# Kernel tuning notes

Hardware: AMD Instinct MI355X
Metric: run time of the kernel (lower is better)

## Reference

```python
import jax, jax.numpy as jnp
import numpy as np

EMBED_DIM = 1024
NUM_HEADS = 16
HEAD_DIM = EMBED_DIM // NUM_HEADS
SCALE = 1.0 / np.sqrt(HEAD_DIM)


def _quant_linear(x, w, b):
    # Per-tensor symmetric int8 quantize -> dequantize -> GEMM (faithful to QuantizedLinear)
    s = jnp.max(jnp.abs(w)) / 127.0
    w_dq = jnp.clip(jnp.round(w / s), -128.0, 127.0) * s
    return jnp.einsum('bse,oe->bso', x, w_dq) + b


def setup_inputs() -> dict:
    key = jax.random.key(0)
    ks = jax.random.split(key, 7)
    B, S, E = 2, 2048, EMBED_DIM
    return {
        'query': jax.random.normal(ks[0], (B, S, E), dtype=jnp.float32),
        'key': jax.random.normal(ks[1], (B, S, E), dtype=jnp.float32),
        'value': jax.random.normal(ks[2], (B, S, E), dtype=jnp.float32),
        'Wq': jax.random.normal(ks[3], (E, E), dtype=jnp.float32) * 0.02,
        'bq': jnp.zeros((E,), dtype=jnp.float32),
        'Wk': jax.random.normal(ks[4], (E, E), dtype=jnp.float32) * 0.02,
        'bk': jnp.zeros((E,), dtype=jnp.float32),
        'Wv': jax.random.normal(ks[5], (E, E), dtype=jnp.float32) * 0.02,
        'bv': jnp.zeros((E,), dtype=jnp.float32),
        'Wo': jax.random.normal(ks[6], (E, E), dtype=jnp.float32) * 0.02,
        'bo': jnp.zeros((E,), dtype=jnp.float32),
    }


def reference(query, key, value, Wq, bq, Wk, bk, Wv, bv, Wo, bo):
    B, S, E = query.shape
    H, D = NUM_HEADS, HEAD_DIM
    Q = _quant_linear(query, Wq, bq).reshape(B, S, H, D).transpose(0, 2, 1, 3)
    K = _quant_linear(key, Wk, bk).reshape(B, S, H, D).transpose(0, 2, 1, 3)
    V = _quant_linear(value, Wv, bv).reshape(B, S, H, D).transpose(0, 2, 1, 3)
    # [B,H,S,S] unfused attention scores
    scores = jnp.einsum('bhqd,bhkd->bhqk', Q, K) * SCALE
    attn = jax.nn.softmax(scores, axis=-1)  # dropout is identity at inference
    out = jnp.einsum('bhqk,bhkd->bhqd', attn, V)
    out = out.transpose(0, 2, 1, 3).reshape(B, S, E)
    return _quant_linear(out, Wo, bo)
```

## Files before the change

kernel.cpp:

```cpp
#include <hip/hip_runtime.h>
#include <math.h>

#define S_LEN 2048
#define EMB   1024
#define NHEAD 16
#define HDIM  64
#define MTOT  4096
#define EXP2_SCALE 0.18033688011112042f

typedef __attribute__((ext_vector_type(8))) short bf16x8;
typedef __attribute__((ext_vector_type(4))) float f32x4;

__device__ __forceinline__ short f2bf(float f) {
  union { float f; unsigned u; } v; v.f = f;
  unsigned r = v.u + 0x7fffu + ((v.u >> 16) & 1u);
  return (short)(r >> 16);
}
__device__ __forceinline__ float bf2f(short s) {
  union { float f; unsigned u; } v; v.u = ((unsigned)(unsigned short)s) << 16;
  return v.f;
}
__device__ __forceinline__ unsigned pkbf(float e0, float e1) {
  unsigned a = __float_as_uint(e1) + 0x8000u;
  unsigned b = __float_as_uint(e0) + 0x8000u;
  return __builtin_amdgcn_perm(a, b, 0x07060302u);
}

__device__ __forceinline__ void gload_lds16(const void* g, void* l) {
  __builtin_amdgcn_global_load_lds(
      (const __attribute__((address_space(1))) void*)g,
      (__attribute__((address_space(3))) void*)l, 16, 0, 0);
}

__global__ void wabsmax_k(const float* __restrict__ W0, const float* __restrict__ W1,
                          const float* __restrict__ W2, const float* __restrict__ W3,
                          unsigned* __restrict__ scaleU) {
  int w = blockIdx.x & 3;
  int part = blockIdx.x >> 2;
  const float* W = (w == 0) ? W0 : (w == 1) ? W1 : (w == 2) ? W2 : W3;
  float m = 0.f;
  int base = part * 16384;
#pragma unroll
  for (int p = 0; p < 16; ++p) {
    const float4 v = *(const float4*)&W[base + p * 1024 + threadIdx.x * 4];
    m = fmaxf(m, fmaxf(fmaxf(fabsf(v.x), fabsf(v.y)), fmaxf(fabsf(v.z), fabsf(v.w))));
  }
  __shared__ float red[256];
  red[threadIdx.x] = m;
  __syncthreads();
  for (int s = 128; s > 0; s >>= 1) {
    if (threadIdx.x < s) red[threadIdx.x] = fmaxf(red[threadIdx.x], red[threadIdx.x + s]);
    __syncthreads();
  }
  if (threadIdx.x == 0) atomicMax(&scaleU[w], __float_as_uint(red[0]));
}

__global__ void wquant_k(const float* __restrict__ W0, const float* __restrict__ W1,
                         const float* __restrict__ W2, const float* __restrict__ W3,
                         short* __restrict__ Q0, short* __restrict__ Q1,
                         short* __restrict__ Q2, short* __restrict__ Q3,
                         const unsigned* __restrict__ scaleU, float* __restrict__ sVal) {
  int w = blockIdx.y;
  const float* W = (w == 0) ? W0 : (w == 1) ? W1 : (w == 2) ? W2 : W3;
  short* Q = (w == 0) ? Q0 : (w == 1) ? Q1 : (w == 2) ? Q2 : Q3;
  float s = __uint_as_float(scaleU[w]) * (1.0f / 127.0f);
  if (blockIdx.x == 0 && threadIdx.x == 0) sVal[w] = s;
  int idx = (blockIdx.x * 256 + threadIdx.x) * 4;
  float4 v = *(const float4*)&W[idx];
  short4 q;
  q.x = f2bf(fminf(fmaxf(rintf(v.x / s), -128.f), 127.f));
  q.y = f2bf(fminf(fmaxf(rintf(v.y / s), -128.f), 127.f));
  q.z = f2bf(fminf(fmaxf(rintf(v.z / s), -128.f), 127.f));
  q.w = f2bf(fminf(fmaxf(rintf(v.w / s), -128.f), 127.f));
  *(short4*)&Q[idx] = q;
}

__global__ void acast_k(const float* __restrict__ A0, const float* __restrict__ A1,
                        const float* __restrict__ A2,
                        short* __restrict__ H0, short* __restrict__ H1,
                        short* __restrict__ H2) {
  int w = blockIdx.y;
  const float* A = (w == 0) ? A0 : (w == 1) ? A1 : A2;
  short* H = (w == 0) ? H0 : (w == 1) ? H1 : H2;
  int idx = (blockIdx.x * 256 + threadIdx.x) * 4;
  float4 v = *(const float4*)&A[idx];
  short4 h;
  h.x = f2bf(v.x); h.y = f2bf(v.y); h.z = f2bf(v.z); h.w = f2bf(v.w);
  *(short4*)&H[idx] = h;
}

__device__ __forceinline__ void gemm_core(
    const short* __restrict__ Ah, const short* __restrict__ Bq, int m0, int n0,
    short* AhS, short* BsS, f32x4 acc[4][4]) {
  const int tid = threadIdx.x;
  const int lane = tid & 63, wave = tid >> 6;
  const int quad = lane >> 4, l16 = lane & 15;
  const int wm = wave >> 1, wn = wave & 1;

  const int swrow = lane >> 2, swcol = (lane & 3) * 8;
  const short* agh = Ah + (m0 + wave * 32 + swrow) * 1024 + swcol;
  const short* bgp = Bq + (n0 + wave * 32 + swrow) * 1024 + swcol;
  short* sA0 = AhS + wave * 1024;
  short* sB0 = BsS + wave * 1024;

  for (int k0 = 0; k0 < 1024; k0 += 32) {
    __syncthreads();
    gload_lds16(agh + k0,             sA0);
    gload_lds16(agh + 16 * 1024 + k0, sA0 + 512);
    gload_lds16(bgp + k0,             sB0);
    gload_lds16(bgp + 16 * 1024 + k0, sB0 + 512);
    __syncthreads();
    bf16x8 ah[4], bb[4];
#pragma unroll
    for (int mi = 0; mi < 4; ++mi) {
      int row = wm * 64 + mi * 16 + l16;
      ah[mi] = *(const bf16x8*)&AhS[row * 32 + quad * 8];
    }
#pragma unroll
    for (int ni = 0; ni < 4; ++ni) {
      int row = wn * 64 + ni * 16 + l16;
      bb[ni] = *(const bf16x8*)&BsS[row * 32 + quad * 8];
    }
#pragma unroll
    for (int mi = 0; mi < 4; ++mi)
#pragma unroll
      for (int ni = 0; ni < 4; ++ni)
        acc[mi][ni] = __builtin_amdgcn_mfma_f32_16x16x32_bf16(ah[mi], bb[ni], acc[mi][ni], 0, 0, 0);
  }
}

__global__ __launch_bounds__(256, 2) void gemm_qkv(
    const short* __restrict__ QA, const short* __restrict__ KA, const short* __restrict__ VA,
    const short* __restrict__ WqQ, const short* __restrict__ WkQ, const short* __restrict__ WvQ,
    const float* __restrict__ sVal,
    const float* __restrict__ bq, const float* __restrict__ bk, const float* __restrict__ bv,
    short* __restrict__ Qh, short* __restrict__ Kh, short* __restrict__ Vh) {
  __shared__ __align__(16) short AhS[128 * 32];
  __shared__ __align__(16) short BsS[128 * 32];
  const int z = blockIdx.z;
  const short* Ah = (z == 0) ? QA : (z == 1) ? KA : VA;
  const short* Bq = (z == 0) ? WqQ : (z == 1) ? WkQ : WvQ;
  const float* bias = (z == 0) ? bq : (z == 1) ? bk : bv;
  short* oh = (z == 0) ? Qh : (z == 1) ? Kh : Vh;

  const int m0 = blockIdx.y * 128, n0 = blockIdx.x * 128;
  f32x4 acc[4][4];
#pragma unroll
  for (int i = 0; i < 4; ++i)
#pragma unroll
    for (int j = 0; j < 4; ++j) acc[i][j] = (f32x4){0.f, 0.f, 0.f, 0.f};

  gemm_core(Ah, Bq, m0, n0, AhS, BsS, acc);

  const int lane = threadIdx.x & 63, wave = threadIdx.x >> 6;
  const int quad = lane >> 4, l16 = lane & 15;
  const int wm = wave >> 1, wn = wave & 1;
  const float s = sVal[z];
#pragma unroll
  for (int mi = 0; mi < 4; ++mi) {
#pragma unroll
    for (int ni = 0; ni < 4; ++ni) {
      int rowb = m0 + wm * 64 + mi * 16 + quad * 4;
      int col = n0 + wn * 64 + ni * 16 + l16;
      float bia = bias[col];
      int h = col >> 6, d = col & 63;
      if (z < 2) {
#pragma unroll
        for (int r = 0; r < 4; ++r) {
          float v = acc[mi][ni][r] * s + bia;
          int row = rowb + r;
          int b = row >> 11, sq = row & 2047;
          oh[((b * 16 + h) * 2048 + sq) * 64 + d] = f2bf(v);
        }
      } else {
        int b = rowb >> 11, sq = rowb & 2047;
        short4 pk;
        pk.x = f2bf(acc[mi][ni][0] * s + bia);
        pk.y = f2bf(acc[mi][ni][1] * s + bia);
        pk.z = f2bf(acc[mi][ni][2] * s + bia);
        pk.w = f2bf(acc[mi][ni][3] * s + bia);
        *(short4*)&oh[((b * 16 + h) * 64 + d) * 2048 + sq] = pk;
      }
    }
  }
}

__global__ __launch_bounds__(256, 2) void gemm_o(
    const short* __restrict__ OAh, const short* __restrict__ OAl,
    const short* __restrict__ WoQ, const float* __restrict__ sPtr,
    const float* __restrict__ bias, float* __restrict__ outF) {
  __shared__ __align__(16) short AhS[128 * 32];
  __shared__ __align__(16) short AlS[128 * 32];
  __shared__ __align__(16) short BsS[64 * 32];
  const int tid = threadIdx.x;
  const int lane = tid & 63, wave = tid >> 6;
  const int quad = lane >> 4, l16 = lane & 15;
  const int m0 = blockIdx.y * 128, n0 = blockIdx.x * 64;

  f32x4 acc[2][4];
#pragma unroll
  for (int i = 0; i < 2; ++i)
#pragma unroll
    for (int j = 0; j < 4; ++j) acc[i][j] = (f32x4){0.f, 0.f, 0.f, 0.f};

  const int swrow = lane >> 2, swcol = (lane & 3) * 8;
  const short* agh = OAh + (m0 + wave * 32 + swrow) * 1024 + swcol;
  const short* agl = OAl + (m0 + wave * 32 + swrow) * 1024 + swcol;
  const short* bgp = WoQ + (n0 + wave * 16 + swrow) * 1024 + swcol;
  short* sA0 = AhS + wave * 1024;
  short* sA1 = AlS + wave * 1024;
  short* sB0 = BsS + wave * 512;

  for (int k0 = 0; k0 < 1024; k0 += 32) {
    __syncthreads();
    gload_lds16(agh + k0,             sA0);
    gload_lds16(agh + 16 * 1024 + k0, sA0 + 512);
    gload_lds16(agl + k0,             sA1);
    gload_lds16(agl + 16 * 1024 + k0, sA1 + 512);
    gload_lds16(bgp + k0,             sB0);
    __syncthreads();
    bf16x8 ah[2], al[2], bb[4];
#pragma unroll
    for (int mi = 0; mi < 2; ++mi) {
      int row = wave * 32 + mi * 16 + l16;
      ah[mi] = *(const bf16x8*)&AhS[row * 32 + quad * 8];
      al[mi] = *(const bf16x8*)&AlS[row * 32 + quad * 8];
    }
#pragma unroll
    for (int ni = 0; ni < 4; ++ni) {
      int row = ni * 16 + l16;
      bb[ni] = *(const bf16x8*)&BsS[row * 32 + quad * 8];
    }
#pragma unroll
    for (int mi = 0; mi < 2; ++mi)
#pragma unroll
      for (int ni = 0; ni < 4; ++ni) {
        acc[mi][ni] = __builtin_amdgcn_mfma_f32_16x16x32_bf16(ah[mi], bb[ni], acc[mi][ni], 0, 0, 0);
        acc[mi][ni] = __builtin_amdgcn_mfma_f32_16x16x32_bf16(al[mi], bb[ni], acc[mi][ni], 0, 0, 0);
      }
  }

  const float s = *sPtr;
#pragma unroll
  for (int mi = 0; mi < 2; ++mi) {
#pragma unroll
    for (int ni = 0; ni < 4; ++ni) {
      int rowb = m0 + wave * 32 + mi * 16 + quad * 4;
      int col = n0 + ni * 16 + l16;
      float bia = bias[col];
#pragma unroll
      for (int r = 0; r < 4; ++r)
        outF[(rowb + r) * 1024 + col] = acc[mi][ni][r] * s + bia;
    }
  }
}

__global__ __launch_bounds__(256, 4) void flash_k(
    const short* __restrict__ Qh, const short* __restrict__ Kh,
    const short* __restrict__ Vh,
    short* __restrict__ Ohi, short* __restrict__ Olo) {
  __shared__ __align__(16) short Khs[64][72];
  __shared__ __align__(16) short Vhs[64][72];

  const int tid = threadIdx.x;
  const int lane = tid & 63, wave = tid >> 6;
  const int quad = lane >> 4, l16 = lane & 15;
  const int bh = blockIdx.y;
  const int b = bh >> 4, h = bh & 15;
  const int q0 = blockIdx.x * 64 + wave * 16;
  const int qkbase = bh * (S_LEN * HDIM);
  const int vbase  = bh * (HDIM * S_LEN);

  const int qrow = qkbase + (q0 + l16) * HDIM;
  const bf16x8 qb0 = *(const bf16x8*)&Qh[qrow + quad * 8];
  const bf16x8 qb1 = *(const bf16x8*)&Qh[qrow + 32 + quad * 8];

  f32x4 zero = {0.f, 0.f, 0.f, 0.f};
  f32x4 oacc[4];
#pragma unroll
  for (int i = 0; i < 4; ++i) oacc[i] = zero;
  float lsum = 0.f;

  const int sr = tid >> 2, sc8 = (tid & 3) * 8;
  const int srP = (sr & 32) | (((sr >> 2) & 1) << 4) | (((sr >> 3) & 3) << 2) | (sr & 3);
  const int kgl = qkbase + sr * HDIM + sc8;
  const int vgl = vbase + sr * S_LEN + sc8;

  bf16x8 pk0 = *(const bf16x8*)&Kh[kgl];
  bf16x8 pk1 = *(const bf16x8*)&Kh[kgl + 32];
  bf16x8 pv0 = *(const bf16x8*)&Vh[vgl];
  bf16x8 pv1 = *(const bf16x8*)&Vh[vgl + 32];

  for (int kt = 0; kt < S_LEN; kt += 64) {
    __syncthreads();
    *(bf16x8*)&Khs[srP][sc8]      = pk0;
    *(bf16x8*)&Khs[srP][sc8 + 32] = pk1;
    *(bf16x8*)&Vhs[sr][sc8]       = pv0;
    *(bf16x8*)&Vhs[sr][sc8 + 32]  = pv1;
    __syncthreads();
    if (kt + 64 < S_LEN) {
      int kg = kgl + (kt + 64) * HDIM;
      int vg = vgl + (kt + 64);
      pk0 = *(const bf16x8*)&Kh[kg];
      pk1 = *(const bf16x8*)&Kh[kg + 32];
      pv0 = *(const bf16x8*)&Vh[vg];
      pv1 = *(const bf16x8*)&Vh[vg + 32];
    }
    f32x4 sc[4];
#pragma unroll
    for (int nj = 0; nj < 4; ++nj) {
      const int kr = nj * 16 + l16;
      bf16x8 kf0 = *(const bf16x8*)&Khs[kr][quad * 8];
      bf16x8 kf1 = *(const bf16x8*)&Khs[kr][32 + quad * 8];
      f32x4 sv = zero;
      sv = __builtin_amdgcn_mfma_f32_16x16x32_bf16(kf0, qb0, sv, 0, 0, 0);
      sv = __builtin_amdgcn_mfma_f32_16x16x32_bf16(kf1, qb1, sv, 0, 0, 0);
      sc[nj] = sv;
    }
#pragma unroll
    for (int nj = 0; nj < 4; ++nj)
#pragma unroll
      for (int r = 0; r < 4; ++r)
        sc[nj][r] = exp2f(sc[nj][r] * EXP2_SCALE);
    float psum = 0.f;
#pragma unroll
    for (int nj = 0; nj < 4; ++nj)
      psum += (sc[nj][0] + sc[nj][1]) + (sc[nj][2] + sc[nj][3]);
    psum += __shfl_xor(psum, 16);
    psum += __shfl_xor(psum, 32);
    lsum += psum;
    union { bf16x8 v; unsigned u[4]; } P0, P1;
    P0.u[0] = pkbf(sc[0][0], sc[0][1]);
    P0.u[1] = pkbf(sc[0][2], sc[0][3]);
    P0.u[2] = pkbf(sc[1][0], sc[1][1]);
    P0.u[3] = pkbf(sc[1][2], sc[1][3]);
    P1.u[0] = pkbf(sc[2][0], sc[2][1]);
    P1.u[1] = pkbf(sc[2][2], sc[2][3]);
    P1.u[2] = pkbf(sc[3][0], sc[3][1]);
    P1.u[3] = pkbf(sc[3][2], sc[3][3]);
#pragma unroll
    for (int ni = 0; ni < 4; ++ni) {
      int vr = ni * 16 + l16;
      bf16x8 vf0 = *(const bf16x8*)&Vhs[vr][quad * 8];
      bf16x8 vf1 = *(const bf16x8*)&Vhs[vr][32 + quad * 8];
      oacc[ni] = __builtin_amdgcn_mfma_f32_16x16x32_bf16(P0.v, vf0, oacc[ni], 0, 0, 0);
      oacc[ni] = __builtin_amdgcn_mfma_f32_16x16x32_bf16(P1.v, vf1, oacc[ni], 0, 0, 0);
    }
  }
#pragma unroll
  for (int r = 0; r < 4; ++r) {
    float inv = 1.f / __shfl(lsum, quad * 4 + r);
    int row = b * S_LEN + q0 + quad * 4 + r;
#pragma unroll
    for (int ni = 0; ni < 4; ++ni) {
      float v = oacc[ni][r] * inv;
      int idx = row * 1024 + h * 64 + ni * 16 + l16;
      short hi = f2bf(v);
      Ohi[idx] = hi;
      Olo[idx] = f2bf(v - bf2f(hi));
    }
  }
}

extern "C" void kernel_launch(void* const* d_in, const int* in_sizes, int n_in,
                              void* d_out, int out_size, void* d_ws, size_t ws_size,
                              hipStream_t stream) {
  const float* query = (const float*)d_in[0];
  const float* key_i = (const float*)d_in[1];
  const float* value = (const float*)d_in[2];
  const float* Wq = (const float*)d_in[3];
  const float* bq = (const float*)d_in[4];
  const float* Wk = (const float*)d_in[5];
  const float* bk = (const float*)d_in[6];
  const float* Wv = (const float*)d_in[7];
  const float* bv = (const float*)d_in[8];
  const float* Wo = (const float*)d_in[9];
  const float* bo = (const float*)d_in[10];
  float* out = (float*)d_out;

  char* w = (char*)d_ws;
  unsigned* scaleU = (unsigned*)w;
  float* sVal = (float*)(w + 256);
  size_t off = 512;
  const size_t SZ_W = 2097152;
  const size_t SZ_A = 8388608;
  short* WqQ = (short*)(w + off); off += SZ_W;
  short* WkQ = (short*)(w + off); off += SZ_W;
  short* WvQ = (short*)(w + off); off += SZ_W;
  short* WoQ = (short*)(w + off); off += SZ_W;
  short* Qa  = (short*)(w + off); off += SZ_A;
  short* Ka  = (short*)(w + off); off += SZ_A;
  short* Va  = (short*)(w + off); off += SZ_A;
  short* Qh  = (short*)(w + off); off += SZ_A;
  short* Kh  = (short*)(w + off); off += SZ_A;
  short* Vh  = (short*)(w + off); off += SZ_A;
  short* Ohi = Qa;
  short* Olo = Ka;

  (void)hipMemsetAsync(scaleU, 0, 16, stream);
  wabsmax_k<<<256, 256, 0, stream>>>(Wq, Wk, Wv, Wo, scaleU);
  wquant_k<<<dim3(1024, 4), 256, 0, stream>>>(Wq, Wk, Wv, Wo, WqQ, WkQ, WvQ, WoQ, scaleU, sVal);
  acast_k<<<dim3(4096, 3), 256, 0, stream>>>(query, key_i, value, Qa, Ka, Va);
  gemm_qkv<<<dim3(8, 32, 3), 256, 0, stream>>>(Qa, Ka, Va, WqQ, WkQ, WvQ, sVal,
                                               bq, bk, bv, Qh, Kh, Vh);
  flash_k<<<dim3(32, 32), 256, 0, stream>>>(Qh, Kh, Vh, Ohi, Olo);
  gemm_o<<<dim3(16, 32), 256, 0, stream>>>(Ohi, Olo, WoQ, sVal + 3, bo, out);
}
```

Before: 268.8 us.

## Process two query groups per wave in flash kernel and fold exp2 scale into Q

Each wave now handles 32 query rows (two 16-row groups) instead of 16, so every K/V fragment read from shared memory feeds twice as many MFMAs, and the grid is halved to 512 blocks. The softmax exp2 scale is folded into the Q projection epilogue, which removes a multiply per score in the attention loop. In exchange the kernel uses more registers (launch bounds lowered to 2 blocks/SM) and has fewer blocks, which may reduce occupancy. Folding the scale before the bf16 rounding of Q slightly changes numerics.

```diff
diff --git a/kernel.cpp b/kernel.cpp
--- a/kernel.cpp
+++ b/kernel.cpp
@@ -155,7 +155,8 @@
   const int lane = threadIdx.x & 63, wave = threadIdx.x >> 6;
   const int quad = lane >> 4, l16 = lane & 15;
   const int wm = wave >> 1, wn = wave & 1;
-  const float s = sVal[z];
+  float s = sVal[z];
+  float post = (z == 0) ? EXP2_SCALE : 1.0f;
 #pragma unroll
   for (int mi = 0; mi < 4; ++mi) {
 #pragma unroll
@@ -167,7 +168,7 @@
       if (z < 2) {
 #pragma unroll
         for (int r = 0; r < 4; ++r) {
-          float v = acc[mi][ni][r] * s + bia;
+          float v = (acc[mi][ni][r] * s + bia) * post;
           int row = rowb + r;
           int b = row >> 11, sq = row & 2047;
           oh[((b * 16 + h) * 2048 + sq) * 64 + d] = f2bf(v);
@@ -255,7 +256,7 @@
   }
 }
 
-__global__ __launch_bounds__(256, 4) void flash_k(
+__global__ __launch_bounds__(256, 2) void flash_k(
     const short* __restrict__ Qh, const short* __restrict__ Kh,
     const short* __restrict__ Vh,
     short* __restrict__ Ohi, short* __restrict__ Olo) {
@@ -267,19 +268,25 @@
   const int quad = lane >> 4, l16 = lane & 15;
   const int bh = blockIdx.y;
   const int b = bh >> 4, h = bh & 15;
-  const int q0 = blockIdx.x * 64 + wave * 16;
+  const int q0 = blockIdx.x * 128 + wave * 32;
   const int qkbase = bh * (S_LEN * HDIM);
   const int vbase  = bh * (HDIM * S_LEN);
 
-  const int qrow = qkbase + (q0 + l16) * HDIM;
-  const bf16x8 qb0 = *(const bf16x8*)&Qh[qrow + quad * 8];
-  const bf16x8 qb1 = *(const bf16x8*)&Qh[qrow + 32 + quad * 8];
+  bf16x8 qb[2][2];
+#pragma unroll
+  for (int g = 0; g < 2; ++g) {
+    const int qrow = qkbase + (q0 + g * 16 + l16) * HDIM;
+    qb[g][0] = *(const bf16x8*)&Qh[qrow + quad * 8];
+    qb[g][1] = *(const bf16x8*)&Qh[qrow + 32 + quad * 8];
+  }
 
   f32x4 zero = {0.f, 0.f, 0.f, 0.f};
-  f32x4 oacc[4];
-#pragma unroll
-  for (int i = 0; i < 4; ++i) oacc[i] = zero;
-  float lsum = 0.f;
+  f32x4 oacc[2][4];
+#pragma unroll
+  for (int g = 0; g < 2; ++g)
+#pragma unroll
+    for (int i = 0; i < 4; ++i) oacc[g][i] = zero;
+  float lsum[2] = {0.f, 0.f};
 
   const int sr = tid >> 2, sc8 = (tid & 3) * 8;
   const int srP = (sr & 32) | (((sr >> 2) & 1) << 4) | (((sr >> 3) & 3) << 2) | (sr & 3);
@@ -306,58 +313,73 @@
       pv0 = *(const bf16x8*)&Vh[vg];
       pv1 = *(const bf16x8*)&Vh[vg + 32];
     }
-    f32x4 sc[4];
+    f32x4 sc[2][4];
 #pragma unroll
     for (int nj = 0; nj < 4; ++nj) {
       const int kr = nj * 16 + l16;
       bf16x8 kf0 = *(const bf16x8*)&Khs[kr][quad * 8];
       bf16x8 kf1 = *(const bf16x8*)&Khs[kr][32 + quad * 8];
-      f32x4 sv = zero;
-      sv = __builtin_amdgcn_mfma_f32_16x16x32_bf16(kf0, qb0, sv, 0, 0, 0);
-      sv = __builtin_amdgcn_mfma_f32_16x16x32_bf16(kf1, qb1, sv, 0, 0, 0);
-      sc[nj] = sv;
-    }
-#pragma unroll
-    for (int nj = 0; nj < 4; ++nj)
-#pragma unroll
-      for (int r = 0; r < 4; ++r)
-        sc[nj][r] = exp2f(sc[nj][r] * EXP2_SCALE);
-    float psum = 0.f;
-#pragma unroll
-    for (int nj = 0; nj < 4; ++nj)
-      psum += (sc[nj][0] + sc[nj][1]) + (sc[nj][2] + sc[nj][3]);
-    psum += __shfl_xor(psum, 16);
-    psum += __shfl_xor(psum, 32);
-    lsum += psum;
-    union { bf16x8 v; unsigned u[4]; } P0, P1;
-    P0.u[0] = pkbf(sc[0][0], sc[0][1]);
-    P0.u[1] = pkbf(sc[0][2], sc[0][3]);
-    P0.u[2] = pkbf(sc[1][0], sc[1][1]);
-    P0.u[3] = pkbf(sc[1][2], sc[1][3]);
-    P1.u[0] = pkbf(sc[2][0], sc[2][1]);
-    P1.u[1] = pkbf(sc[2][2], sc[2][3]);
-    P1.u[2] = pkbf(sc[3][0], sc[3][1]);
-    P1.u[3] = pkbf(sc[3][2], sc[3][3]);
+#pragma unroll
+      for (int g = 0; g < 2; ++g) {
+        f32x4 sv = zero;
+        sv = __builtin_amdgcn_mfma_f32_16x16x32_bf16(kf0, qb[g][0], sv, 0, 0, 0);
+        sv = __builtin_amdgcn_mfma_f32_16x16x32_bf16(kf1, qb[g][1], sv, 0, 0, 0);
+        sc[g][nj] = sv;
+      }
+    }
+#pragma unroll
+    for (int g = 0; g < 2; ++g) {
+#pragma unroll
+      for (int nj = 0; nj < 4; ++nj)
+#pragma unroll
+        for (int r = 0; r < 4; ++r)
+          sc[g][nj][r] = exp2f(sc[g][nj][r]);
+      float psum = 0.f;
+#pragma unroll
+      for (int nj = 0; nj < 4; ++nj)
+        psum += (sc[g][nj][0] + sc[g][nj][1]) + (sc[g][nj][2] + sc[g][nj][3]);
+      psum += __shfl_xor(psum, 16);
+      psum += __shfl_xor(psum, 32);
+      lsum[g] += psum;
+    }
+    union { bf16x8 v; unsigned u[4]; } P[2][2];
+#pragma unroll
+    for (int g = 0; g < 2; ++g) {
+      P[g][0].u[0] = pkbf(sc[g][0][0], sc[g][0][1]);
+      P[g][0].u[1] = pkbf(sc[g][0][2], sc[g][0][3]);
+      P[g][0].u[2] = pkbf(sc[g][1][0], sc[g][1][1]);
+      P[g][0].u[3] = pkbf(sc[g][1][2], sc[g][1][3]);
+      P[g][1].u[0] = pkbf(sc[g][2][0], sc[g][2][1]);
+      P[g][1].u[1] = pkbf(sc[g][2][2], sc[g][2][3]);
+      P[g][1].u[2] = pkbf(sc[g][3][0], sc[g][3][1]);
+      P[g][1].u[3] = pkbf(sc[g][3][2], sc[g][3][3]);
+    }
 #pragma unroll
     for (int ni = 0; ni < 4; ++ni) {
       int vr = ni * 16 + l16;
       bf16x8 vf0 = *(const bf16x8*)&Vhs[vr][quad * 8];
       bf16x8 vf1 = *(const bf16x8*)&Vhs[vr][32 + quad * 8];
-      oacc[ni] = __builtin_amdgcn_mfma_f32_16x16x32_bf16(P0.v, vf0, oacc[ni], 0, 0, 0);
-      oacc[ni] = __builtin_amdgcn_mfma_f32_16x16x32_bf16(P1.v, vf1, oacc[ni], 0, 0, 0);
-    }
-  }
-#pragma unroll
-  for (int r = 0; r < 4; ++r) {
-    float inv = 1.f / __shfl(lsum, quad * 4 + r);
-    int row = b * S_LEN + q0 + quad * 4 + r;
-#pragma unroll
-    for (int ni = 0; ni < 4; ++ni) {
-      float v = oacc[ni][r] * inv;
-      int idx = row * 1024 + h * 64 + ni * 16 + l16;
-      short hi = f2bf(v);
-      Ohi[idx] = hi;
-      Olo[idx] = f2bf(v - bf2f(hi));
+#pragma unroll
+      for (int g = 0; g < 2; ++g) {
+        oacc[g][ni] = __builtin_amdgcn_mfma_f32_16x16x32_bf16(P[g][0].v, vf0, oacc[g][ni], 0, 0, 0);
+        oacc[g][ni] = __builtin_amdgcn_mfma_f32_16x16x32_bf16(P[g][1].v, vf1, oacc[g][ni], 0, 0, 0);
+      }
+    }
+  }
+#pragma unroll
+  for (int g = 0; g < 2; ++g) {
+#pragma unroll
+    for (int r = 0; r < 4; ++r) {
+      float inv = 1.f / __shfl(lsum[g], quad * 4 + r);
+      int row = b * S_LEN + q0 + g * 16 + quad * 4 + r;
+#pragma unroll
+      for (int ni = 0; ni < 4; ++ni) {
+        float v = oacc[g][ni][r] * inv;
+        int idx = row * 1024 + h * 64 + ni * 16 + l16;
+        short hi = f2bf(v);
+        Ohi[idx] = hi;
+        Olo[idx] = f2bf(v - bf2f(hi));
+      }
     }
   }
 }
@@ -403,6 +425,6 @@
   acast_k<<<dim3(4096, 3), 256, 0, stream>>>(query, key_i, value, Qa, Ka, Va);
   gemm_qkv<<<dim3(8, 32, 3), 256, 0, stream>>>(Qa, Ka, Va, WqQ, WkQ, WvQ, sVal,
                                                bq, bk, bv, Qh, Kh, Vh);
-  flash_k<<<dim3(32, 32), 256, 0, stream>>>(Qh, Kh, Vh, Ohi, Olo);
+  flash_k<<<dim3(16, 32), 256, 0, stream>>>(Qh, Kh, Vh, Ohi, Olo);
   gemm_o<<<dim3(16, 32), 256, 0, stream>>>(Ohi, Olo, WoQ, sVal + 3, bo, out);
 }
```

Measured after the change: 257.2 us. 4.3% less time.
